# Kernel optimization log

Hardware: AMD Instinct MI355X
Metric: run time of the kernel (lower is better)

Reference implementation:

```python
import jax, jax.numpy as jnp
import numpy as np

D_EMB = 1024
B, T = 8, 2048

def setup_inputs() -> dict:
    key = jax.random.key(0)
    ks = jax.random.split(key, 7)
    s = 0.02
    return {
        "x": jax.random.normal(ks[0], (B, T, D_EMB), dtype=jnp.float32),
        "W_attn": jax.random.normal(ks[1], (3 * D_EMB, D_EMB), dtype=jnp.float32) * s,
        "b_attn": jax.random.normal(ks[2], (3 * D_EMB,), dtype=jnp.float32) * s,
        "W_proj": jax.random.normal(ks[3], (D_EMB, D_EMB), dtype=jnp.float32) * s,
        "b_proj": jax.random.normal(ks[4], (D_EMB,), dtype=jnp.float32) * s,
        "W_fc": jax.random.normal(ks[5], (1, D_EMB), dtype=jnp.float32) * s,
        "b_fc": jax.random.normal(ks[6], (1,), dtype=jnp.float32) * s,
    }

def reference(x, W_attn, b_attn, W_proj, b_proj, W_fc, b_fc):
    # qkv projection: torch Linear => x @ W.T + b
    qkv = jnp.einsum('btc,dc->btd', x, W_attn) + b_attn          # [B,T,3C]
    q, k, v = jnp.split(qkv, 3, axis=2)                          # each [B,T,C]
    scale = q.shape[-1] ** (-0.5)
    attn_scores = jnp.einsum('btc,bsc->bts', q, k) * scale       # [B,T,T]
    attn_weights = jax.nn.softmax(attn_scores, axis=-1)          # traditional softmax
    y = jnp.einsum('bts,bsc->btc', attn_weights, v)              # [B,T,C]
    y = jnp.einsum('btc,dc->btd', y, W_proj) + b_proj            # [B,T,C]
    out = jnp.einsum('btc,oc->bto', y, W_fc) + b_fc              # [B,T,1]
    return out
```

## Files before the change

### kernel.cpp

```cpp
#include <hip/hip_runtime.h>
#include <stdint.h>

#define D_EMB 1024
#define NBATCH 8
#define SEQ 2048
#define MTOT (NBATCH*SEQ)

typedef __attribute__((ext_vector_type(8))) short short8;
typedef __attribute__((ext_vector_type(4))) float f32x4;

__device__ __forceinline__ ushort bf16r(float x) {
  union { float f; uint32_t u; } c; c.f = x;
  return (ushort)((c.u + 0x7fffu + ((c.u >> 16) & 1u)) >> 16);
}

__device__ __forceinline__ void cp16(const ushort* g, ushort* l) {
  __builtin_amdgcn_global_load_lds(
      (const __attribute__((address_space(1))) void*)g,
      (__attribute__((address_space(3))) void*)l, 16, 0, 0);
}

__global__ void cvt_kernel(const float4* __restrict__ in, ushort* __restrict__ out, long n4) {
  long i = blockIdx.x * (long)blockDim.x + threadIdx.x;
  long stride = (long)gridDim.x * blockDim.x;
  for (; i < n4; i += stride) {
    float4 v = in[i];
    ushort4 o = make_ushort4(bf16r(v.x), bf16r(v.y), bf16r(v.z), bf16r(v.w));
    *(ushort4*)(out + i * 4) = o;
  }
}

__global__ __launch_bounds__(256) void cvt_x_vw(
    const float4* __restrict__ x, const float4* __restrict__ wv_eff4,
    const float* __restrict__ sc, ushort* __restrict__ xb, float* __restrict__ vw) {
  long row = blockIdx.x;
  int tid = threadIdx.x;
  float4 v = x[row * 256 + tid];
  float4 w = wv_eff4[tid];
  ushort4 o = make_ushort4(bf16r(v.x), bf16r(v.y), bf16r(v.z), bf16r(v.w));
  *(ushort4*)(xb + row * D_EMB + tid * 4) = o;
  float s = v.x * w.x + v.y * w.y + v.z * w.z + v.w * w.w;
  int lane = tid & 63, wv0 = tid >> 6;
  #pragma unroll
  for (int off = 32; off; off >>= 1) s += __shfl_xor(s, off);
  __shared__ float red[4];
  if (lane == 0) red[wv0] = s;
  __syncthreads();
  if (tid == 0) vw[row] = red[0] + red[1] + red[2] + red[3] + sc[1];
}

__global__ void init_kernel(const float* __restrict__ bp, const float* __restrict__ Wfc,
                            const float* __restrict__ bfc,
                            float* __restrict__ w_eff, float* __restrict__ wv_eff,
                            float* __restrict__ numden, float* __restrict__ sc) {
  int tid = threadIdx.x;
  int b = blockIdx.x;
  if (b == 0) { w_eff[tid] = 0.f; return; }
  if (b == 1) { wv_eff[tid] = 0.f; return; }
  if (b >= 3) { numden[(long)(b - 3) * 1024 + tid] = 0.f; return; }
  float v = bp[tid] * Wfc[tid];
  int lane = tid & 63, w = tid >> 6;
  #pragma unroll
  for (int off = 32; off; off >>= 1) v += __shfl_xor(v, off);
  __shared__ float red[16];
  if (lane == 0) red[w] = v;
  __syncthreads();
  if (tid == 0) {
    float s = 0.f;
    #pragma unroll
    for (int i = 0; i < 16; i++) s += red[i];
    sc[0] = s + bfc[0];
  }
}

__global__ void prep1(const float* __restrict__ Wp, const float* __restrict__ Wfc,
                      float* __restrict__ w_eff) {
  int c = blockIdx.x * 256 + threadIdx.x;
  int d0 = blockIdx.y * 64;
  float s = 0.f;
  #pragma unroll 8
  for (int d = d0; d < d0 + 64; d++) s += Wfc[d] * Wp[(long)d * D_EMB + c];
  atomicAdd(&w_eff[c], s);
}

__global__ void sc1_kernel(const float* __restrict__ battn, const float* __restrict__ w_eff,
                           float* __restrict__ sc) {
  int tid = threadIdx.x;
  float v = battn[2048 + tid] * w_eff[tid];
  int lane = tid & 63, w = tid >> 6;
  #pragma unroll
  for (int off = 32; off; off >>= 1) v += __shfl_xor(v, off);
  __shared__ float red[16];
  if (lane == 0) red[w] = v;
  __syncthreads();
  if (tid == 0) {
    float s = 0.f;
    #pragma unroll
    for (int i = 0; i < 16; i++) s += red[i];
    sc[1] = s;
  }
}

__global__ void prep2(const float* __restrict__ Wattn, const float* __restrict__ w_eff,
                      float* __restrict__ wv_eff) {
  int d = blockIdx.x * 256 + threadIdx.x;
  int c0 = blockIdx.y * 64;
  float s = 0.f;
  #pragma unroll 8
  for (int c = c0; c < c0 + 64; c++) s += w_eff[c] * Wattn[(long)(2048 + c) * D_EMB + d];
  atomicAdd(&wv_eff[d], s);
}

template<bool FUSED>
__global__ __launch_bounds__(256, 3) void gemm_nt(
    const ushort* __restrict__ A, long lda, long sAz,
    const ushort* __restrict__ B, long ldb, long sBz,
    ushort* __restrict__ C, long ldc,
    const float* __restrict__ bias, float scale, int K,
    const float* __restrict__ vw, float* __restrict__ num, float* __restrict__ den) {
  __shared__ __align__(16) ushort lds_a[128 * 32];
  __shared__ __align__(16) ushort lds_b[128 * 32];
  int z = blockIdx.z;
  const ushort* Az = A + (long)z * sAz;
  const ushort* Bz = B + (long)z * sBz;
  long m0 = (long)blockIdx.y * 128, n0 = (long)blockIdx.x * 128;
  int t = threadIdx.x;
  int wave = t >> 6, lane = t & 63;
  int r = lane & 15, q = lane >> 4;
  int wm = (wave & 1) * 64, wn = (wave >> 1) * 64;

  f32x4 acc[4][4] = {};

  int row0 = t >> 2;
  int kc = ((t & 3) - ((row0 >> 1) & 3)) & 3;
  const ushort* Ap0 = Az + (m0 + row0) * lda + kc * 8;
  const ushort* Ap1 = Az + (m0 + row0 + 64) * lda + kc * 8;
  const ushort* Bp0 = Bz + (n0 + row0) * ldb + kc * 8;
  const ushort* Bp1 = Bz + (n0 + row0 + 64) * ldb + kc * 8;

  int swzr = (r >> 1) & 3;

  #pragma unroll 1
  for (int k0 = 0; k0 < K; k0 += 32) {
    if (k0) __syncthreads();
    cp16(Ap0 + k0, lds_a + t * 8);
    cp16(Ap1 + k0, lds_a + (t + 256) * 8);
    cp16(Bp0 + k0, lds_b + t * 8);
    cp16(Bp1 + k0, lds_b + (t + 256) * 8);
    __syncthreads();
    short8 af[4], bf[4];
    int ks = ((q + swzr) & 3);
    #pragma unroll
    for (int i = 0; i < 4; i++)
      af[i] = *(const short8*)(lds_a + ((wm + i * 16 + r) * 4 + ks) * 8);
    #pragma unroll
    for (int j = 0; j < 4; j++)
      bf[j] = *(const short8*)(lds_b + ((wn + j * 16 + r) * 4 + ks) * 8);
    #pragma unroll
    for (int i = 0; i < 4; i++)
      #pragma unroll
      for (int j = 0; j < 4; j++)
        acc[i][j] = __builtin_amdgcn_mfma_f32_16x16x32_bf16(af[i], bf[j], acc[i][j], 0, 0, 0);
  }

  if (!FUSED) {
    #pragma unroll
    for (int i = 0; i < 4; i++) {
      #pragma unroll
      for (int j = 0; j < 4; j++) {
        long col = n0 + wn + j * 16 + r;
        float bj = bias[col];
        #pragma unroll
        for (int rr = 0; rr < 4; rr++) {
          long row = m0 + wm + i * 16 + q * 4 + rr;
          C[row * ldc + col] = bf16r(acc[i][j][rr] * scale + bj);
        }
      }
    }
  } else {
    const float* vwz = vw + (long)z * SEQ + n0;
    float* numz = num + (long)z * SEQ + m0;
    float* denz = den + (long)z * SEQ + m0;
    float vwj[4];
    #pragma unroll
    for (int j = 0; j < 4; j++) vwj[j] = vwz[wn + j * 16 + r];
    #pragma unroll
    for (int i = 0; i < 4; i++) {
      #pragma unroll
      for (int rr = 0; rr < 4; rr++) {
        float sn = 0.f, sd = 0.f;
        #pragma unroll
        for (int j = 0; j < 4; j++) {
          float e = __expf(acc[i][j][rr] * scale);
          sd += e;
          sn += e * vwj[j];
        }
        #pragma unroll
        for (int off = 1; off < 16; off <<= 1) {
          sn += __shfl_xor(sn, off);
          sd += __shfl_xor(sd, off);
        }
        if (r == 0) {
          int row = wm + i * 16 + q * 4 + rr;
          atomicAdd(&numz[row], sn);
          atomicAdd(&denz[row], sd);
        }
      }
    }
  }
}

__global__ __launch_bounds__(256) void finalize(
    const float* __restrict__ num, const float* __restrict__ den,
    const float* __restrict__ sc, float* __restrict__ out) {
  long i = blockIdx.x * 256L + threadIdx.x;
  out[i] = num[i] / den[i] + sc[0];
}

extern "C" void kernel_launch(void* const* d_in, const int* in_sizes, int n_in,
                              void* d_out, int out_size, void* d_ws, size_t ws_size,
                              hipStream_t stream) {
  const float* x     = (const float*)d_in[0];
  const float* Wattn = (const float*)d_in[1];
  const float* battn = (const float*)d_in[2];
  const float* Wproj = (const float*)d_in[3];
  const float* bproj = (const float*)d_in[4];
  const float* Wfc   = (const float*)d_in[5];
  const float* bfc   = (const float*)d_in[6];
  float* out = (float*)d_out;

  const size_t OFF_XB    = 0;
  const size_t OFF_WQKB  = 33554432;
  const size_t OFF_QK    = 37748736;
  const size_t OFF_NUM   = 104857600;
  const size_t OFF_DEN   = 104923136;
  const size_t OFF_VW    = 104988672;
  const size_t OFF_WEFF  = 105054208;
  const size_t OFF_WVEFF = 105058304;
  const size_t OFF_SC    = 105062400;
  const size_t NEED      = 105062408;
  if (ws_size < NEED) return;

  char* ws = (char*)d_ws;
  ushort* xb    = (ushort*)(ws + OFF_XB);
  ushort* wqkb  = (ushort*)(ws + OFF_WQKB);
  ushort* qk    = (ushort*)(ws + OFF_QK);
  float* num    = (float*)(ws + OFF_NUM);
  float* den    = (float*)(ws + OFF_DEN);
  float* vw     = (float*)(ws + OFF_VW);
  float* w_eff  = (float*)(ws + OFF_WEFF);
  float* wv_eff = (float*)(ws + OFF_WVEFF);
  float* sc     = (float*)(ws + OFF_SC);

  init_kernel<<<dim3(35), dim3(1024), 0, stream>>>(bproj, Wfc, bfc, w_eff, wv_eff, num, sc);
  prep1<<<dim3(4, 16), dim3(256), 0, stream>>>(Wproj, Wfc, w_eff);
  sc1_kernel<<<dim3(1), dim3(1024), 0, stream>>>(battn, w_eff, sc);
  prep2<<<dim3(4, 16), dim3(256), 0, stream>>>(Wattn, w_eff, wv_eff);

  cvt_kernel<<<dim3(2048), dim3(256), 0, stream>>>((const float4*)Wattn, wqkb, (long)2048 * D_EMB / 4);
  cvt_x_vw<<<dim3(MTOT), dim3(256), 0, stream>>>((const float4*)x, (const float4*)wv_eff, sc, xb, vw);

  gemm_nt<false><<<dim3(16, 128, 1), dim3(256), 0, stream>>>(
      xb, (long)D_EMB, 0L, wqkb, (long)D_EMB, 0L,
      qk, 2048L, battn, 1.0f, D_EMB, nullptr, nullptr, nullptr);

  gemm_nt<true><<<dim3(16, 16, NBATCH), dim3(256), 0, stream>>>(
      qk, 2048L, (long)SEQ * 2048, qk + 1024, 2048L, (long)SEQ * 2048,
      nullptr, 0L, nullptr, 0.03125f, D_EMB, vw, num, den);

  finalize<<<dim3(64), dim3(256), 0, stream>>>(num, den, sc, out);
}
```

Before: 307.6 us.

## Double GEMM K-tile to 64 with XOR swizzle, merge prep kernels, row-per-wave conversion

The GEMM K-step grows from 32 to 64, using a new XOR-based LDS swizzle and two MFMA sub-steps per barrier pair. This halves the number of sync and load rounds but doubles LDS use, and the occupancy hint is raised to 4 blocks. The prep kernels use more, smaller blocks, and the sc1 kernel is folded into prep2 to drop one launch. The x conversion now handles one row per wave, which removes the shared-memory reduction and the block barrier.

```diff
diff --git a/kernel.cpp b/kernel.cpp
--- a/kernel.cpp
+++ b/kernel.cpp
@@ -31,22 +31,24 @@
 }
 
 __global__ __launch_bounds__(256) void cvt_x_vw(
-    const float4* __restrict__ x, const float4* __restrict__ wv_eff4,
+    const float4* __restrict__ x4, const float4* __restrict__ wv4,
     const float* __restrict__ sc, ushort* __restrict__ xb, float* __restrict__ vw) {
-  long row = blockIdx.x;
-  int tid = threadIdx.x;
-  float4 v = x[row * 256 + tid];
-  float4 w = wv_eff4[tid];
-  ushort4 o = make_ushort4(bf16r(v.x), bf16r(v.y), bf16r(v.z), bf16r(v.w));
-  *(ushort4*)(xb + row * D_EMB + tid * 4) = o;
-  float s = v.x * w.x + v.y * w.y + v.z * w.z + v.w * w.w;
-  int lane = tid & 63, wv0 = tid >> 6;
+  int wave = threadIdx.x >> 6, lane = threadIdx.x & 63;
+  long row = (long)blockIdx.x * 4 + wave;
+  const float4* xr = x4 + row * 256;
+  ushort* xo = xb + row * D_EMB;
+  float s = 0.f;
+  #pragma unroll
+  for (int i = 0; i < 4; i++) {
+    int idx = lane + i * 64;
+    float4 v = xr[idx];
+    float4 w = wv4[idx];
+    *(ushort4*)(xo + idx * 4) = make_ushort4(bf16r(v.x), bf16r(v.y), bf16r(v.z), bf16r(v.w));
+    s += v.x * w.x + v.y * w.y + v.z * w.z + v.w * w.w;
+  }
   #pragma unroll
   for (int off = 32; off; off >>= 1) s += __shfl_xor(s, off);
-  __shared__ float red[4];
-  if (lane == 0) red[wv0] = s;
-  __syncthreads();
-  if (tid == 0) vw[row] = red[0] + red[1] + red[2] + red[3] + sc[1];
+  if (lane == 0) vw[row] = s + sc[1];
 }
 
 __global__ void init_kernel(const float* __restrict__ bp, const float* __restrict__ Wfc,
@@ -76,50 +78,48 @@
 __global__ void prep1(const float* __restrict__ Wp, const float* __restrict__ Wfc,
                       float* __restrict__ w_eff) {
   int c = blockIdx.x * 256 + threadIdx.x;
-  int d0 = blockIdx.y * 64;
+  int d0 = blockIdx.y * 16;
   float s = 0.f;
-  #pragma unroll 8
-  for (int d = d0; d < d0 + 64; d++) s += Wfc[d] * Wp[(long)d * D_EMB + c];
+  #pragma unroll
+  for (int d = d0; d < d0 + 16; d++) s += Wfc[d] * Wp[(long)d * D_EMB + c];
   atomicAdd(&w_eff[c], s);
 }
 
-__global__ void sc1_kernel(const float* __restrict__ battn, const float* __restrict__ w_eff,
-                           float* __restrict__ sc) {
+__global__ void prep2(const float* __restrict__ Wattn, const float* __restrict__ battn,
+                      const float* __restrict__ w_eff, float* __restrict__ wv_eff,
+                      float* __restrict__ sc) {
   int tid = threadIdx.x;
-  float v = battn[2048 + tid] * w_eff[tid];
-  int lane = tid & 63, w = tid >> 6;
-  #pragma unroll
-  for (int off = 32; off; off >>= 1) v += __shfl_xor(v, off);
-  __shared__ float red[16];
-  if (lane == 0) red[w] = v;
-  __syncthreads();
-  if (tid == 0) {
-    float s = 0.f;
-    #pragma unroll
-    for (int i = 0; i < 16; i++) s += red[i];
-    sc[1] = s;
-  }
-}
-
-__global__ void prep2(const float* __restrict__ Wattn, const float* __restrict__ w_eff,
-                      float* __restrict__ wv_eff) {
-  int d = blockIdx.x * 256 + threadIdx.x;
-  int c0 = blockIdx.y * 64;
+  if (blockIdx.y == 64) {
+    if (blockIdx.x != 0) return;
+    float v = 0.f;
+    #pragma unroll
+    for (int i = 0; i < 4; i++) { int c = tid + i * 256; v += battn[2048 + c] * w_eff[c]; }
+    int lane = tid & 63, w = tid >> 6;
+    #pragma unroll
+    for (int off = 32; off; off >>= 1) v += __shfl_xor(v, off);
+    __shared__ float red[4];
+    if (lane == 0) red[w] = v;
+    __syncthreads();
+    if (tid == 0) sc[1] = red[0] + red[1] + red[2] + red[3];
+    return;
+  }
+  int d = blockIdx.x * 256 + tid;
+  int c0 = blockIdx.y * 16;
   float s = 0.f;
-  #pragma unroll 8
-  for (int c = c0; c < c0 + 64; c++) s += w_eff[c] * Wattn[(long)(2048 + c) * D_EMB + d];
+  #pragma unroll
+  for (int c = c0; c < c0 + 16; c++) s += w_eff[c] * Wattn[(long)(2048 + c) * D_EMB + d];
   atomicAdd(&wv_eff[d], s);
 }
 
 template<bool FUSED>
-__global__ __launch_bounds__(256, 3) void gemm_nt(
+__global__ __launch_bounds__(256, 4) void gemm_nt(
     const ushort* __restrict__ A, long lda, long sAz,
     const ushort* __restrict__ B, long ldb, long sBz,
     ushort* __restrict__ C, long ldc,
     const float* __restrict__ bias, float scale, int K,
     const float* __restrict__ vw, float* __restrict__ num, float* __restrict__ den) {
-  __shared__ __align__(16) ushort lds_a[128 * 32];
-  __shared__ __align__(16) ushort lds_b[128 * 32];
+  __shared__ __align__(16) ushort lds_a[128 * 64];
+  __shared__ __align__(16) ushort lds_b[128 * 64];
   int z = blockIdx.z;
   const ushort* Az = A + (long)z * sAz;
   const ushort* Bz = B + (long)z * sBz;
@@ -131,36 +131,42 @@
 
   f32x4 acc[4][4] = {};
 
-  int row0 = t >> 2;
-  int kc = ((t & 3) - ((row0 >> 1) & 3)) & 3;
-  const ushort* Ap0 = Az + (m0 + row0) * lda + kc * 8;
-  const ushort* Ap1 = Az + (m0 + row0 + 64) * lda + kc * 8;
-  const ushort* Bp0 = Bz + (n0 + row0) * ldb + kc * 8;
-  const ushort* Bp1 = Bz + (n0 + row0 + 64) * ldb + kc * 8;
-
-  int swzr = (r >> 1) & 3;
+  int row0 = t >> 3;
+  int kc = (t & 7) ^ (row0 & 7);
+  const ushort* Ap = Az + (m0 + row0) * lda + kc * 8;
+  const ushort* Bp = Bz + (n0 + row0) * ldb + kc * 8;
+  long a32 = 32 * lda, b32 = 32 * ldb;
+
+  int swz = r & 7;
 
   #pragma unroll 1
-  for (int k0 = 0; k0 < K; k0 += 32) {
+  for (int k0 = 0; k0 < K; k0 += 64) {
     if (k0) __syncthreads();
-    cp16(Ap0 + k0, lds_a + t * 8);
-    cp16(Ap1 + k0, lds_a + (t + 256) * 8);
-    cp16(Bp0 + k0, lds_b + t * 8);
-    cp16(Bp1 + k0, lds_b + (t + 256) * 8);
+    cp16(Ap + k0,            lds_a + t * 8);
+    cp16(Ap + k0 + a32,      lds_a + (t + 256) * 8);
+    cp16(Ap + k0 + 2 * a32,  lds_a + (t + 512) * 8);
+    cp16(Ap + k0 + 3 * a32,  lds_a + (t + 768) * 8);
+    cp16(Bp + k0,            lds_b + t * 8);
+    cp16(Bp + k0 + b32,      lds_b + (t + 256) * 8);
+    cp16(Bp + k0 + 2 * b32,  lds_b + (t + 512) * 8);
+    cp16(Bp + k0 + 3 * b32,  lds_b + (t + 768) * 8);
     __syncthreads();
-    short8 af[4], bf[4];
-    int ks = ((q + swzr) & 3);
-    #pragma unroll
-    for (int i = 0; i < 4; i++)
-      af[i] = *(const short8*)(lds_a + ((wm + i * 16 + r) * 4 + ks) * 8);
-    #pragma unroll
-    for (int j = 0; j < 4; j++)
-      bf[j] = *(const short8*)(lds_b + ((wn + j * 16 + r) * 4 + ks) * 8);
-    #pragma unroll
-    for (int i = 0; i < 4; i++)
+    #pragma unroll
+    for (int kk = 0; kk < 2; kk++) {
+      int cidx = (kk * 4 + q) ^ swz;
+      short8 af[4], bf[4];
+      #pragma unroll
+      for (int i = 0; i < 4; i++)
+        af[i] = *(const short8*)(lds_a + ((wm + i * 16 + r) * 8 + cidx) * 8);
       #pragma unroll
       for (int j = 0; j < 4; j++)
-        acc[i][j] = __builtin_amdgcn_mfma_f32_16x16x32_bf16(af[i], bf[j], acc[i][j], 0, 0, 0);
+        bf[j] = *(const short8*)(lds_b + ((wn + j * 16 + r) * 8 + cidx) * 8);
+      #pragma unroll
+      for (int i = 0; i < 4; i++)
+        #pragma unroll
+        for (int j = 0; j < 4; j++)
+          acc[i][j] = __builtin_amdgcn_mfma_f32_16x16x32_bf16(af[i], bf[j], acc[i][j], 0, 0, 0);
+    }
   }
 
   if (!FUSED) {
@@ -253,12 +259,11 @@
   float* sc     = (float*)(ws + OFF_SC);
 
   init_kernel<<<dim3(35), dim3(1024), 0, stream>>>(bproj, Wfc, bfc, w_eff, wv_eff, num, sc);
-  prep1<<<dim3(4, 16), dim3(256), 0, stream>>>(Wproj, Wfc, w_eff);
-  sc1_kernel<<<dim3(1), dim3(1024), 0, stream>>>(battn, w_eff, sc);
-  prep2<<<dim3(4, 16), dim3(256), 0, stream>>>(Wattn, w_eff, wv_eff);
+  prep1<<<dim3(4, 64), dim3(256), 0, stream>>>(Wproj, Wfc, w_eff);
+  prep2<<<dim3(4, 65), dim3(256), 0, stream>>>(Wattn, battn, w_eff, wv_eff, sc);
 
   cvt_kernel<<<dim3(2048), dim3(256), 0, stream>>>((const float4*)Wattn, wqkb, (long)2048 * D_EMB / 4);
-  cvt_x_vw<<<dim3(MTOT), dim3(256), 0, stream>>>((const float4*)x, (const float4*)wv_eff, sc, xb, vw);
+  cvt_x_vw<<<dim3(4096), dim3(256), 0, stream>>>((const float4*)x, (const float4*)wv_eff, sc, xb, vw);
 
   gemm_nt<false><<<dim3(16, 128, 1), dim3(256), 0, stream>>>(
       xb, (long)D_EMB, 0L, wqkb, (long)D_EMB, 0L,
```

Measured after the change: 271.3 us. -11.8%, faster.
